# Performance work log

Hardware: AMD Instinct MI355X
Metric: run time of the kernel (lower is better)

Reference implementation:

```python
import jax, jax.numpy as jnp
import numpy as np

MAX_GRAD = 200.0
N_BLOCKS = 8

@jax.custom_jvp
def sqrt_bound(x):
    return jnp.sqrt(x)

@sqrt_bound.defjvp
def _sqrt_bound_jvp(primals, tangents):
    (x,), (xd,) = primals, tangents
    clipped = jnp.maximum(x, 1.0 / (4.0 * MAX_GRAD * MAX_GRAD))
    return jnp.sqrt(x), xd / (2.0 * jnp.sqrt(clipped))

def block_diag_linear(x, W, b):
    # x: [B,S,Din], W: [n_blocks, Din/n, Dout/n], b: [Dout]
    B, S, Din = x.shape
    n, blk_in, blk_out = W.shape
    xb = x.reshape(B, S, n, blk_in)
    y = jnp.einsum('bsnh,nhd->bsnd', xb, W).reshape(B, S, n * blk_out)
    return y + b

def _scan_combine(c1, c2):
    a1r, a1i, x1r, x1i = c1
    a2r, a2i, x2r, x2i = c2
    ar = a2r * a1r - a2i * a1i
    ai = a2r * a1i + a2i * a1r
    xr = a2r * x1r - a2i * x1i + x2r
    xi = a2r * x1i + a2i * x1r + x2i
    return (ar, ai, xr, xi)

def rglru_forward(x, a_real_param, a_imag_param, W_in, b_in, Wg_x, bg_x, Wg_a, bg_a, W_out, b_out):
    # x: [B, S, d_in]
    x_h = jnp.einsum('bsd,dh->bsh', x, W_in) + b_in          # [B,S,d_hidden]
    gate_x = jax.nn.sigmoid(block_diag_linear(x_h, Wg_x, bg_x))  # [B,S,Dh]
    gate_a = jax.nn.sigmoid(block_diag_linear(x_h, Wg_a, bg_a))  # [B,S,Dh]
    log_a = -8.0 * gate_a * jax.nn.softplus(a_real_param)        # Re(log a)
    log_a_imag = a_imag_param * gate_a                           # Im(log a)
    mag = jnp.exp(log_a)
    a_re = mag * jnp.cos(log_a_imag)
    a_im = mag * jnp.sin(log_a_imag)
    a_sq = jnp.exp(2.0 * log_a)                                  # |a|^2
    Dh = log_a.shape[-1]
    # merged_to_complex: first half -> real part, second half -> imag part
    xr = x_h[..., :Dh]
    xi = x_h[..., Dh:]
    xr = gate_x * xr
    xi = gate_x * xi
    norm = sqrt_bound(1.0 - a_sq)                                # input normalization
    xr = norm * xr
    xi = norm * xi
    # linear recurrence h_t = a_t * h_{t-1} + x_t  (h0 = 0), parallel scan over seq axis
    _, _, hr, hi = jax.lax.associative_scan(_scan_combine, (a_re, a_im, xr, xi), axis=1)
    h = jnp.concatenate([hr, hi], axis=-1)                       # complex_to_merged
    h_last = jnp.concatenate([hr[:, -1], hi[:, -1]], axis=-1)    # [B, d_hidden]
    y = jnp.einsum('bsh,hd->bsd', h, W_out) + b_out              # Dense(d_in)
    return y, h_last

def setup_inputs() -> dict:
    key = jax.random.key(0)
    ks = jax.random.split(key, 10)
    B, S, d_in, d_hidden = 4, 4096, 2048, 2048
    Dh = d_hidden // 2
    blk_in, blk_out = d_hidden // N_BLOCKS, Dh // N_BLOCKS
    r_min, r_max, max_imag, eps = 0.9, 0.999, 0.1, 1e-8
    u1 = jax.random.uniform(ks[0], (Dh,))
    a_real = 0.5 * jnp.log(u1 * (r_max**2 - r_min**2) + r_min**2 + eps)
    a_real_param = jnp.log(jnp.exp(-a_real) - 1.0)
    a_imag_param = jnp.pi * max_imag * jax.random.uniform(ks[1], (Dh,))
    x = jax.random.normal(ks[2], (B, S, d_in), dtype=jnp.float32)
    W_in = jax.random.normal(ks[3], (d_in, d_hidden)) / np.sqrt(d_in)
    Wg_x = jax.random.normal(ks[4], (N_BLOCKS, blk_in, blk_out)) / np.sqrt(blk_in)
    Wg_a = jax.random.normal(ks[5], (N_BLOCKS, blk_in, blk_out)) / np.sqrt(blk_in)
    W_out = jax.random.normal(ks[6], (d_hidden, d_in)) / np.sqrt(d_hidden)
    return {
        'x': x,
        'a_real_param': a_real_param.astype(jnp.float32),
        'a_imag_param': a_imag_param.astype(jnp.float32),
        'W_in': W_in.astype(jnp.float32), 'b_in': jnp.zeros((d_hidden,), jnp.float32),
        'Wg_x': Wg_x.astype(jnp.float32), 'bg_x': jnp.zeros((Dh,), jnp.float32),
        'Wg_a': Wg_a.astype(jnp.float32), 'bg_a': jnp.zeros((Dh,), jnp.float32),
        'W_out': W_out.astype(jnp.float32), 'b_out': jnp.zeros((d_in,), jnp.float32),
    }

def reference(x, a_real_param, a_imag_param, W_in, b_in, Wg_x, bg_x, Wg_a, bg_a, W_out, b_out):
    return rglru_forward(x, a_real_param, a_imag_param, W_in, b_in, Wg_x, bg_x, Wg_a, bg_a, W_out, b_out)
```

## Files before the change

### kernel.cpp

```cpp
#include <hip/hip_runtime.h>
#include <hip/hip_bf16.h>


typedef unsigned short u16;
typedef unsigned int u32;
typedef unsigned long long u64;
typedef __attribute__((ext_vector_type(8))) short short8;
typedef __attribute__((ext_vector_type(4))) float floatx4;

#define DEV __device__ __forceinline__

DEV float bf2f(u16 u) { union { u32 i; float f; } v; v.i = ((u32)u) << 16; return v.f; }
DEV u16 f2bf(float f) {
  union { float f; u32 i; } v; v.f = f;
  u32 r = v.i + 0x7fffu + ((v.i >> 16) & 1u);
  return (u16)(r >> 16);
}
DEV float sigmoidf_(float x) { return 1.f / (1.f + __expf(-x)); }

#if __has_builtin(__builtin_amdgcn_global_load_lds)
#define USE_ASYNC_LDS 1
#endif

DEV void cp16(const void* g, void* l) {
#if defined(USE_ASYNC_LDS) && defined(__HIP_DEVICE_COMPILE__)
  __builtin_amdgcn_global_load_lds((const __attribute__((address_space(1))) u32*)g,
                                   (__attribute__((address_space(3))) u32*)l, 16, 0, 0);
#else
  *(short8*)l = *(const short8*)g;
#endif
}
#define WAIT_VM() asm volatile("s_waitcnt vmcnt(0)" ::: "memory")

__global__ __launch_bounds__(256) void convert_f32_bf16(
    const float* __restrict__ src, u16* __restrict__ dst, long n) {
  long i = ((long)blockIdx.x * 256 + threadIdx.x) * 8;
  if (i >= n) return;
  float4 a = *(const float4*)(src + i);
  float4 b = *(const float4*)(src + i + 4);
  union { u16 u[8]; short8 v; } o;
  o.u[0] = f2bf(a.x); o.u[1] = f2bf(a.y); o.u[2] = f2bf(a.z); o.u[3] = f2bf(a.w);
  o.u[4] = f2bf(b.x); o.u[5] = f2bf(b.y); o.u[6] = f2bf(b.z); o.u[7] = f2bf(b.w);
  *(short8*)(dst + i) = o.v;
}

__global__ __launch_bounds__(256) void transpose_f32_bf16(
    const float* __restrict__ src, u16* __restrict__ dst, int R, int C,
    long sBatch, long dBatch) {
  __shared__ u16 tile[32][33];
  const int n = blockIdx.z;
  src += (long)n * sBatch;
  dst += (long)n * dBatch;
  const int c0 = blockIdx.x * 32, r0 = blockIdx.y * 32;
  const int tx = threadIdx.x, ty = threadIdx.y;
#pragma unroll
  for (int i = 0; i < 32; i += 8)
    tile[ty + i][tx] = f2bf(src[(long)(r0 + ty + i) * C + c0 + tx]);
  __syncthreads();
#pragma unroll
  for (int i = 0; i < 32; i += 8) dst[(long)(c0 + ty + i) * R + r0 + tx] = tile[tx][ty + i];
}

#define MQ(MH, NH)                                                                   \
  {                                                                                  \
    _Pragma("unroll") for (int mi = 0; mi < 4; ++mi)                                 \
        _Pragma("unroll") for (int nj = 0; nj < 2; ++nj) {                           \
      acc[(MH)*4 + mi][(NH)*2 + nj] = __builtin_amdgcn_mfma_f32_16x16x32_bf16(       \
          af[(MH)*4 + mi][0], bf[(NH)*2 + nj][0], acc[(MH)*4 + mi][(NH)*2 + nj],     \
          0, 0, 0);                                                                  \
      acc[(MH)*4 + mi][(NH)*2 + nj] = __builtin_amdgcn_mfma_f32_16x16x32_bf16(       \
          af[(MH)*4 + mi][1], bf[(NH)*2 + nj][1], acc[(MH)*4 + mi][(NH)*2 + nj],     \
          0, 0, 0);                                                                  \
    }                                                                                \
  }

#define AOFF(mi, k2) ((((wr << 7) + ((mi) << 4) + lm) << 6) + (((((k2) << 2) + lq) ^ sz) << 3))
#define BOFF(nj, k2) ((((wc << 6) + ((nj) << 4) + lm) << 6) + (((((k2) << 2) + lq) ^ sz) << 3))

template <typename OutT>
__global__ __launch_bounds__(512, 2) void gemm256_bt_bias(
    const u16* __restrict__ A, const u16* __restrict__ BT,
    const float* __restrict__ bias, OutT* __restrict__ C, int M, int N, int K) {
  __shared__ __align__(16) u16 As[2 * 16384];
  __shared__ __align__(16) u16 Bs[2 * 16384];
  const int mt = M >> 8;
  const int cpx = gridDim.x >> 3;
  const int bid = blockIdx.x;
  const int wg = (bid & 7) * cpx + (bid >> 3);
  const int bm = wg % mt, bn = wg / mt;
  const int m0 = bm << 8, n0 = bn << 8;
  const int tid = threadIdx.x;
  const int lane = tid & 63, wid = tid >> 6;
  const int wr = wid >> 2, wc = wid & 3;
  const int lq = lane >> 4, lm = lane & 15;
  const int sz = lm & 7;
  const int NT = K >> 6;

  auto stage = [&](int h) {
    int t = h >> 2, j = h & 3;
    const u16* src;
    u16* dst;
    if (j < 2) { src = A + (size_t)(m0 + (j << 7)) * K; dst = As; }
    else       { src = BT + (size_t)(n0 + ((j & 1) << 7)) * K; dst = Bs; }
    dst += ((t & 1) << 14) + ((j & 1) << 13);
    const size_t kb = (size_t)(t << 6);
#pragma unroll
    for (int l = 0; l < 2; ++l) {
      int slot = (l << 9) + tid;
      int row = slot >> 3;
      int gch = (slot & 7) ^ (row & 7);
      cp16(src + (size_t)row * K + kb + (gch << 3), (char*)dst + slot * 16);
    }
  };

  floatx4 acc[8][4];
#pragma unroll
  for (int i = 0; i < 8; ++i)
#pragma unroll
    for (int j = 0; j < 4; ++j) { acc[i][j].x = 0.f; acc[i][j].y = 0.f; acc[i][j].z = 0.f; acc[i][j].w = 0.f; }
  short8 af[8][2], bf[4][2];

#pragma unroll
  for (int h = 0; h < 7; ++h)
    if (h < 4 * NT) stage(h);
  asm volatile("s_waitcnt vmcnt(6)" ::: "memory");
  __builtin_amdgcn_s_barrier();

  for (int T = 0; T < NT; ++T) {
    const u16* Asb = As + ((T & 1) << 14);
    const u16* Bsb = Bs + ((T & 1) << 14);
    const int hb = (T << 2) + 7;
#pragma unroll
    for (int mi = 0; mi < 8; ++mi) {
      af[mi][0] = *(const short8*)(Asb + AOFF(mi, 0));
      af[mi][1] = *(const short8*)(Asb + AOFF(mi, 1));
    }
#pragma unroll
    for (int nj = 0; nj < 2; ++nj) {
      bf[nj][0] = *(const short8*)(Bsb + BOFF(nj, 0));
      bf[nj][1] = *(const short8*)(Bsb + BOFF(nj, 1));
    }
    if (hb < 4 * NT) stage(hb);
    __builtin_amdgcn_s_barrier();
    asm volatile("s_waitcnt lgkmcnt(0)" ::: "memory");
    __builtin_amdgcn_sched_barrier(0);
    __builtin_amdgcn_s_setprio(1);
    MQ(0, 0);
    __builtin_amdgcn_s_setprio(0);
    __builtin_amdgcn_s_barrier();
#pragma unroll
    for (int nj = 2; nj < 4; ++nj) {
      bf[nj][0] = *(const short8*)(Bsb + BOFF(nj, 0));
      bf[nj][1] = *(const short8*)(Bsb + BOFF(nj, 1));
    }
    if (hb + 1 < 4 * NT) stage(hb + 1);
    __builtin_amdgcn_s_barrier();
    asm volatile("s_waitcnt lgkmcnt(0)" ::: "memory");
    __builtin_amdgcn_sched_barrier(0);
    __builtin_amdgcn_s_setprio(1);
    MQ(0, 1);
    __builtin_amdgcn_s_setprio(0);
    __builtin_amdgcn_s_barrier();
    if (hb + 2 < 4 * NT) stage(hb + 2);
    __builtin_amdgcn_s_barrier();
    __builtin_amdgcn_s_setprio(1);
    MQ(1, 0);
    __builtin_amdgcn_s_setprio(0);
    __builtin_amdgcn_s_barrier();
    if (hb + 3 < 4 * NT) stage(hb + 3);
    __builtin_amdgcn_s_barrier();
    __builtin_amdgcn_s_setprio(1);
    MQ(1, 1);
    __builtin_amdgcn_s_setprio(0);
    if (T == NT - 2) { asm volatile("s_waitcnt vmcnt(0)" ::: "memory"); }
    else if (T < NT - 2) { asm volatile("s_waitcnt vmcnt(6)" ::: "memory"); }
    __builtin_amdgcn_s_barrier();
  }

  float bv[4];
#pragma unroll
  for (int nj = 0; nj < 4; ++nj) bv[nj] = bias[n0 + (wc << 6) + nj * 16 + lm];
  float* Cs = (float*)As;
#pragma unroll
  for (int s = 0; s < 4; ++s) {
    __syncthreads();
    if (wr == (s >> 1)) {
#pragma unroll
      for (int mi2 = 0; mi2 < 4; ++mi2) {
        const int mi = ((s & 1) << 2) + mi2;
#pragma unroll
        for (int nj = 0; nj < 4; ++nj)
#pragma unroll
          for (int rr = 0; rr < 4; ++rr)
            Cs[(mi2 * 16 + lq * 4 + rr) * 256 + (wc << 6) + nj * 16 + lm] =
                acc[mi][nj][rr] + bv[nj];
      }
    }
    __syncthreads();
#pragma unroll
    for (int w = 0; w < 8; ++w) {
      int fi = (w << 9) + tid;
      int rl = fi >> 6, cc = fi & 63;
      float4 v = *(const float4*)&Cs[rl * 256 + (cc << 2)];
      size_t grow = (size_t)(m0 + (s << 6) + rl) * N + n0 + (cc << 2);
      if constexpr (sizeof(OutT) == 2) {
        union { u16 u[4]; u64 q; } o;
        o.u[0] = f2bf(v.x); o.u[1] = f2bf(v.y); o.u[2] = f2bf(v.z); o.u[3] = f2bf(v.w);
        *(u64*)((u16*)C + grow) = o.q;
      } else {
        *(float4*)((float*)C + grow) = v;
      }
    }
  }
}

__global__ __launch_bounds__(256, 2) void gate_elem_kernel(
    const u16* __restrict__ xh, const u16* __restrict__ wgt,
    const float* __restrict__ bgx, const float* __restrict__ bga,
    const float* __restrict__ arp,
    float* __restrict__ ga_out, u16* __restrict__ xr_out, u16* __restrict__ xi_out) {
  __shared__ __align__(16) u16 As[128 * 64];
  __shared__ __align__(16) u16 Bs[256 * 64];

  const int m0 = blockIdx.x << 7;
  const int blk = blockIdx.y;
  const int tid = threadIdx.x;
  const int lane = tid & 63, wid = tid >> 6;
  const int wm = (wid & 1) << 6, wn = (wid >> 1) << 6;
  const int lq = lane >> 4, lm = lane & 15;

  floatx4 acc[4][8];
#pragma unroll
  for (int i = 0; i < 4; ++i)
#pragma unroll
    for (int j = 0; j < 8; ++j) { acc[i][j].x = 0.f; acc[i][j].y = 0.f; acc[i][j].z = 0.f; acc[i][j].w = 0.f; }

  const u16* Ag = xh + (size_t)m0 * 2048 + blk * 256;
  const u16* Bg = wgt + (size_t)blk * 65536;

  for (int kt = 0; kt < 256; kt += 64) {
#pragma unroll
    for (int j = 0; j < 4; ++j) {
      int slot = (j << 8) + tid;
      int row = slot >> 3, ch = slot & 7;
      int gch = ch ^ (row & 7);
      cp16(Ag + (size_t)row * 2048 + kt + (gch << 3), (char*)As + slot * 16);
    }
#pragma unroll
    for (int j = 0; j < 8; ++j) {
      int slot = (j << 8) + tid;
      int row = slot >> 3, ch = slot & 7;
      int gch = ch ^ (row & 7);
      cp16(Bg + (size_t)row * 256 + kt + (gch << 3), (char*)Bs + slot * 16);
    }
    WAIT_VM();
    __syncthreads();
#pragma unroll
    for (int kk = 0; kk < 64; kk += 32) {
      const int lc = (kk >> 3) + lq;
      short8 af[4], bfr[8];
#pragma unroll
      for (int mi = 0; mi < 4; ++mi) {
        int r = wm + mi * 16 + lm;
        af[mi] = *(const short8*)&As[r * 64 + ((lc ^ (r & 7)) << 3)];
      }
#pragma unroll
      for (int ni = 0; ni < 8; ++ni) {
        int r = (ni < 4) ? (wn + ni * 16 + lm) : (128 + wn + (ni - 4) * 16 + lm);
        bfr[ni] = *(const short8*)&Bs[r * 64 + ((lc ^ (r & 7)) << 3)];
      }
#pragma unroll
      for (int mi = 0; mi < 4; ++mi)
#pragma unroll
        for (int ni = 0; ni < 8; ++ni)
          acc[mi][ni] = __builtin_amdgcn_mfma_f32_16x16x32_bf16(af[mi], bfr[ni], acc[mi][ni], 0, 0, 0);
    }
    __syncthreads();
  }

#pragma unroll
  for (int ni = 0; ni < 4; ++ni) {
    const int c = (blk << 7) + wn + ni * 16 + lm;
    const float bxv = bgx[c], bav = bga[c];
    const float sp = log1pf(__expf(arp[c]));
#pragma unroll
    for (int mi = 0; mi < 4; ++mi) {
      const size_t rowg0 = (size_t)m0 + wm + mi * 16 + lq * 4;
#pragma unroll
      for (int r = 0; r < 4; ++r) {
        const size_t rowg = rowg0 + r;
        float gxv = sigmoidf_(acc[mi][ni][r] + bxv);
        float gav = sigmoidf_(acc[mi][ni + 4][r] + bav);
        float mag = __expf(-8.f * gav * sp);
        float norm = sqrtf(fmaxf(1.f - mag * mag, 0.f));
        float f = norm * gxv;
        ga_out[rowg * 1024 + c] = gav;
        xr_out[rowg * 1024 + c] = f2bf(f * bf2f(xh[rowg * 2048 + c]));
        xi_out[rowg * 1024 + c] = f2bf(f * bf2f(xh[rowg * 2048 + 1024 + c]));
      }
    }
  }
}

__global__ __launch_bounds__(256) void scan_pass1(
    const float* __restrict__ ga, const u16* __restrict__ xr, const u16* __restrict__ xi,
    const float* __restrict__ arp, const float* __restrict__ aip,
    float* __restrict__ Ar, float* __restrict__ Ai,
    float* __restrict__ Xr, float* __restrict__ Xi) {
  int tid = blockIdx.x * 256 + threadIdx.x;
  int c = tid & 1023;
  int chunk = (tid >> 10) & 63;
  int b = tid >> 16;
  float sp = log1pf(__expf(arp[c]));
  float aim = aip[c];
  size_t base = ((size_t)b * 4096 + chunk * 64) * 1024 + c;
  float Arr = 1.f, Aii = 0.f, Xrr = 0.f, Xii = 0.f;
#pragma unroll 4
  for (int i = 0; i < 64; ++i) {
    size_t idx = base + (size_t)i * 1024;
    float g = ga[idx];
    float mag = __expf(-8.f * g * sp);
    float s, co;
    __sincosf(aim * g, &s, &co);
    float ar = mag * co, ai = mag * s;
    float nxr = ar * Xrr - ai * Xii + bf2f(xr[idx]);
    float nxi = ar * Xii + ai * Xrr + bf2f(xi[idx]);
    Xrr = nxr; Xii = nxi;
    float nar = ar * Arr - ai * Aii;
    float nai = ar * Aii + ai * Arr;
    Arr = nar; Aii = nai;
  }
  Ar[tid] = Arr; Ai[tid] = Aii; Xr[tid] = Xrr; Xi[tid] = Xii;
}

__global__ __launch_bounds__(256) void scan_pass2(
    const float* __restrict__ Ar, const float* __restrict__ Ai,
    const float* __restrict__ Xr, const float* __restrict__ Xi,
    float* __restrict__ Hr, float* __restrict__ Hi) {
  int tid = blockIdx.x * 256 + threadIdx.x;
  int c = tid & 1023, b = tid >> 10;
  float hr = 0.f, hi = 0.f;
  for (int j = 0; j < 64; ++j) {
    int idx = (b << 16) + (j << 10) + c;
    Hr[idx] = hr; Hi[idx] = hi;
    float ar = Ar[idx], ai = Ai[idx];
    float nhr = ar * hr - ai * hi + Xr[idx];
    float nhi = ar * hi + ai * hr + Xi[idx];
    hr = nhr; hi = nhi;
  }
}

__global__ __launch_bounds__(256) void scan_pass3(
    const float* __restrict__ ga, const u16* __restrict__ xr, const u16* __restrict__ xi,
    const float* __restrict__ arp, const float* __restrict__ aip,
    const float* __restrict__ Hr, const float* __restrict__ Hi,
    u16* __restrict__ h_out, float* __restrict__ tail) {
  int tid = blockIdx.x * 256 + threadIdx.x;
  int c = tid & 1023;
  int chunk = (tid >> 10) & 63;
  int b = tid >> 16;
  float sp = log1pf(__expf(arp[c]));
  float aim = aip[c];
  size_t row0 = (size_t)b * 4096 + chunk * 64;
  size_t base = row0 * 1024 + c;
  float hr = Hr[tid], hi = Hi[tid];
#pragma unroll 4
  for (int i = 0; i < 64; ++i) {
    size_t idx = base + (size_t)i * 1024;
    float g = ga[idx];
    float mag = __expf(-8.f * g * sp);
    float s, co;
    __sincosf(aim * g, &s, &co);
    float ar = mag * co, ai = mag * s;
    float nhr = ar * hr - ai * hi + bf2f(xr[idx]);
    float nhi = ar * hi + ai * hr + bf2f(xi[idx]);
    hr = nhr; hi = nhi;
    size_t r = row0 + i;
    h_out[r * 2048 + c] = f2bf(hr);
    h_out[r * 2048 + 1024 + c] = f2bf(hi);
  }
  if (chunk == 63) {
    tail[(size_t)b * 2048 + c] = hr;
    tail[(size_t)b * 2048 + 1024 + c] = hi;
  }
}

static const size_t OFF_XH = 0;
static const size_t OFF_GA = 67108864;
static const size_t OFF_XR = 134217728;
static const size_t OFF_XI = 167772160;
static const size_t OFF_WIT = 201326592;
static const size_t OFF_WOT = 209715200;
static const size_t OFF_WGT = 218103808;
static const size_t OFF_AGR = 219152384;
static const size_t OFF_AGI = 220200960;
static const size_t OFF_AXR = 221249536;
static const size_t OFF_AXI = 222298112;
static const size_t OFF_HPR = 223346688;
static const size_t OFF_HPI = 224395264;

extern "C" void kernel_launch(void* const* d_in, const int* in_sizes, int n_in,
                              void* d_out, int out_size, void* d_ws, size_t ws_size,
                              hipStream_t stream) {
  const float* x    = (const float*)d_in[0];
  const float* arp  = (const float*)d_in[1];
  const float* aip  = (const float*)d_in[2];
  const float* W_in = (const float*)d_in[3];
  const float* b_in = (const float*)d_in[4];
  const float* Wg_x = (const float*)d_in[5];
  const float* bg_x = (const float*)d_in[6];
  const float* Wg_a = (const float*)d_in[7];
  const float* bg_a = (const float*)d_in[8];
  const float* W_out = (const float*)d_in[9];
  const float* b_out = (const float*)d_in[10];

  char* ws = (char*)d_ws;
  u16* XH = (u16*)(ws + OFF_XH);
  u16* XB = (u16*)(ws + OFF_GA);
  float* GA = (float*)(ws + OFF_GA);
  u16* XR = (u16*)(ws + OFF_XR);
  u16* XI = (u16*)(ws + OFF_XI);
  u16* WIT = (u16*)(ws + OFF_WIT);
  u16* WOT = (u16*)(ws + OFF_WOT);
  u16* WGT = (u16*)(ws + OFF_WGT);
  float* AGR = (float*)(ws + OFF_AGR);
  float* AGI = (float*)(ws + OFF_AGI);
  float* AXR = (float*)(ws + OFF_AXR);
  float* AXI = (float*)(ws + OFF_AXI);
  float* HPR = (float*)(ws + OFF_HPR);
  float* HPI = (float*)(ws + OFF_HPI);

  float* y_out = (float*)d_out;
  float* h_last = (float*)d_out + (size_t)16384 * 2048;

  convert_f32_bf16<<<16384, 256, 0, stream>>>(x, XB, (long)16384 * 2048);

  dim3 tb(32, 8);
  transpose_f32_bf16<<<dim3(64, 64, 1), tb, 0, stream>>>(W_in, WIT, 2048, 2048, 0, 0);
  transpose_f32_bf16<<<dim3(64, 64, 1), tb, 0, stream>>>(W_out, WOT, 2048, 2048, 0, 0);
  transpose_f32_bf16<<<dim3(4, 8, 8), tb, 0, stream>>>(Wg_x, WGT, 256, 128, 32768, 65536);
  transpose_f32_bf16<<<dim3(4, 8, 8), tb, 0, stream>>>(Wg_a, WGT + 32768, 256, 128, 32768, 65536);

  gemm256_bt_bias<u16><<<512, 512, 0, stream>>>(XB, WIT, b_in, XH, 16384, 2048, 2048);
  gate_elem_kernel<<<dim3(128, 8), 256, 0, stream>>>(XH, WGT, bg_x, bg_a, arp, GA, XR, XI);
  scan_pass1<<<1024, 256, 0, stream>>>(GA, XR, XI, arp, aip, AGR, AGI, AXR, AXI);
  scan_pass2<<<16, 256, 0, stream>>>(AGR, AGI, AXR, AXI, HPR, HPI);
  scan_pass3<<<1024, 256, 0, stream>>>(GA, XR, XI, arp, aip, HPR, HPI, XH , h_last);
  gemm256_bt_bias<float><<<512, 512, 0, stream>>>(XH, WOT, b_out, y_out, 16384, 2048, 2048);
}
```

Baseline: 731.1 us.

## Software-pipeline LDS fragment reads across GEMM quarter-steps and pad epilogue stride

Restructures the 256x256 GEMM main loop so LDS fragment reads for the next quadrant, and for the next k-tile, are issued while the current MFMA quadrant runs. Global-to-LDS staging of half-tiles is reordered and the vmcnt waits are adjusted to match. The epilogue staging buffer row stride is padded from 256 to 260 floats to reduce LDS bank conflicts. The intent is to hide LDS read latency behind MFMA work, at the cost of more complex wait and barrier accounting that could introduce races if the counts are wrong.

```diff
diff --git a/kernel.cpp b/kernel.cpp
--- a/kernel.cpp
+++ b/kernel.cpp
@@ -31,6 +31,7 @@
 #endif
 }
 #define WAIT_VM() asm volatile("s_waitcnt vmcnt(0)" ::: "memory")
+#define LGKM0()  do { asm volatile("s_waitcnt lgkmcnt(0)" ::: "memory"); __builtin_amdgcn_sched_barrier(0); } while (0)
 
 __global__ __launch_bounds__(256) void convert_f32_bf16(
     const float* __restrict__ src, u16* __restrict__ dst, long n) {
@@ -77,12 +78,28 @@
 #define AOFF(mi, k2) ((((wr << 7) + ((mi) << 4) + lm) << 6) + (((((k2) << 2) + lq) ^ sz) << 3))
 #define BOFF(nj, k2) ((((wc << 6) + ((nj) << 4) + lm) << 6) + (((((k2) << 2) + lq) ^ sz) << 3))
 
+#define RD_A4(m0_, p)                                                   \
+  {                                                                     \
+    _Pragma("unroll") for (int mi = (m0_); mi < (m0_) + 4; ++mi) {      \
+      af[mi][0] = *(const short8*)((p) + AOFF(mi, 0));                  \
+      af[mi][1] = *(const short8*)((p) + AOFF(mi, 1));                  \
+    }                                                                   \
+  }
+#define RD_B2(n0_, p)                                                   \
+  {                                                                     \
+    _Pragma("unroll") for (int nj = (n0_); nj < (n0_) + 2; ++nj) {      \
+      bf[nj][0] = *(const short8*)((p) + BOFF(nj, 0));                  \
+      bf[nj][1] = *(const short8*)((p) + BOFF(nj, 1));                  \
+    }                                                                   \
+  }
+
 template <typename OutT>
 __global__ __launch_bounds__(512, 2) void gemm256_bt_bias(
     const u16* __restrict__ A, const u16* __restrict__ BT,
     const float* __restrict__ bias, OutT* __restrict__ C, int M, int N, int K) {
-  __shared__ __align__(16) u16 As[2 * 16384];
-  __shared__ __align__(16) u16 Bs[2 * 16384];
+  __shared__ __align__(16) u16 SM[65536];
+  u16* As = SM;
+  u16* Bs = SM + 32768;
   const int mt = M >> 8;
   const int cpx = gridDim.x >> 3;
   const int bid = blockIdx.x;
@@ -96,8 +113,7 @@
   const int sz = lm & 7;
   const int NT = K >> 6;
 
-  auto stage = [&](int h) {
-    int t = h >> 2, j = h & 3;
+  auto stageH = [&](int t, int j) {
     const u16* src;
     u16* dst;
     if (j < 2) { src = A + (size_t)(m0 + (j << 7)) * K; dst = As; }
@@ -120,67 +136,61 @@
     for (int j = 0; j < 4; ++j) { acc[i][j].x = 0.f; acc[i][j].y = 0.f; acc[i][j].z = 0.f; acc[i][j].w = 0.f; }
   short8 af[8][2], bf[4][2];
 
-#pragma unroll
-  for (int h = 0; h < 7; ++h)
-    if (h < 4 * NT) stage(h);
+  stageH(0, 0); stageH(0, 2); stageH(0, 1); stageH(0, 3);
+  stageH(1, 0); stageH(1, 2); stageH(1, 1);
   asm volatile("s_waitcnt vmcnt(6)" ::: "memory");
   __builtin_amdgcn_s_barrier();
+  RD_A4(0, As);
+  RD_B2(0, Bs);
 
   for (int T = 0; T < NT; ++T) {
-    const u16* Asb = As + ((T & 1) << 14);
-    const u16* Bsb = Bs + ((T & 1) << 14);
-    const int hb = (T << 2) + 7;
-#pragma unroll
-    for (int mi = 0; mi < 8; ++mi) {
-      af[mi][0] = *(const short8*)(Asb + AOFF(mi, 0));
-      af[mi][1] = *(const short8*)(Asb + AOFF(mi, 1));
-    }
-#pragma unroll
-    for (int nj = 0; nj < 2; ++nj) {
-      bf[nj][0] = *(const short8*)(Bsb + BOFF(nj, 0));
-      bf[nj][1] = *(const short8*)(Bsb + BOFF(nj, 1));
-    }
-    if (hb < 4 * NT) stage(hb);
-    __builtin_amdgcn_s_barrier();
-    asm volatile("s_waitcnt lgkmcnt(0)" ::: "memory");
-    __builtin_amdgcn_sched_barrier(0);
+    const u16* ca = As + ((T & 1) << 14);
+    const u16* cb = Bs + ((T & 1) << 14);
+    const u16* na = As + (((T + 1) & 1) << 14);
+    const u16* nb = Bs + (((T + 1) & 1) << 14);
+    const bool haveN1 = (T + 1 < NT), haveN2 = (T + 2 < NT);
+    if (haveN1) stageH(T + 1, 3);
+    __builtin_amdgcn_s_barrier();
+    LGKM0();
+    RD_B2(2, cb);
     __builtin_amdgcn_s_setprio(1);
     MQ(0, 0);
     __builtin_amdgcn_s_setprio(0);
     __builtin_amdgcn_s_barrier();
-#pragma unroll
-    for (int nj = 2; nj < 4; ++nj) {
-      bf[nj][0] = *(const short8*)(Bsb + BOFF(nj, 0));
-      bf[nj][1] = *(const short8*)(Bsb + BOFF(nj, 1));
-    }
-    if (hb + 1 < 4 * NT) stage(hb + 1);
-    __builtin_amdgcn_s_barrier();
-    asm volatile("s_waitcnt lgkmcnt(0)" ::: "memory");
-    __builtin_amdgcn_sched_barrier(0);
+    if (haveN2) stageH(T + 2, 0);
+    __builtin_amdgcn_s_barrier();
+    LGKM0();
+    RD_A4(4, ca);
     __builtin_amdgcn_s_setprio(1);
     MQ(0, 1);
     __builtin_amdgcn_s_setprio(0);
-    __builtin_amdgcn_s_barrier();
-    if (hb + 2 < 4 * NT) stage(hb + 2);
-    __builtin_amdgcn_s_barrier();
+    if (T < NT - 2) { asm volatile("s_waitcnt vmcnt(8)" ::: "memory"); }
+    else            { asm volatile("s_waitcnt vmcnt(0)" ::: "memory"); }
+    __builtin_amdgcn_s_barrier();
+    if (haveN2) stageH(T + 2, 2);
+    __builtin_amdgcn_s_barrier();
+    LGKM0();
+    if (haveN1) RD_A4(0, na);
     __builtin_amdgcn_s_setprio(1);
     MQ(1, 0);
     __builtin_amdgcn_s_setprio(0);
-    __builtin_amdgcn_s_barrier();
-    if (hb + 3 < 4 * NT) stage(hb + 3);
-    __builtin_amdgcn_s_barrier();
+    if (T < NT - 2) { asm volatile("s_waitcnt vmcnt(4)" ::: "memory"); }
+    else            { asm volatile("s_waitcnt vmcnt(0)" ::: "memory"); }
+    __builtin_amdgcn_s_barrier();
+    if (haveN2) stageH(T + 2, 1);
+    __builtin_amdgcn_s_barrier();
+    LGKM0();
+    if (haveN1) RD_B2(0, nb);
     __builtin_amdgcn_s_setprio(1);
     MQ(1, 1);
     __builtin_amdgcn_s_setprio(0);
-    if (T == NT - 2) { asm volatile("s_waitcnt vmcnt(0)" ::: "memory"); }
-    else if (T < NT - 2) { asm volatile("s_waitcnt vmcnt(6)" ::: "memory"); }
     __builtin_amdgcn_s_barrier();
   }
 
   float bv[4];
 #pragma unroll
   for (int nj = 0; nj < 4; ++nj) bv[nj] = bias[n0 + (wc << 6) + nj * 16 + lm];
-  float* Cs = (float*)As;
+  float* Cs = (float*)SM;
 #pragma unroll
   for (int s = 0; s < 4; ++s) {
     __syncthreads();
@@ -192,7 +202,7 @@
         for (int nj = 0; nj < 4; ++nj)
 #pragma unroll
           for (int rr = 0; rr < 4; ++rr)
-            Cs[(mi2 * 16 + lq * 4 + rr) * 256 + (wc << 6) + nj * 16 + lm] =
+            Cs[(mi2 * 16 + lq * 4 + rr) * 260 + (wc << 6) + nj * 16 + lm] =
                 acc[mi][nj][rr] + bv[nj];
       }
     }
@@ -201,7 +211,7 @@
     for (int w = 0; w < 8; ++w) {
       int fi = (w << 9) + tid;
       int rl = fi >> 6, cc = fi & 63;
-      float4 v = *(const float4*)&Cs[rl * 256 + (cc << 2)];
+      float4 v = *(const float4*)&Cs[rl * 260 + (cc << 2)];
       size_t grow = (size_t)(m0 + (s << 6) + rl) * N + n0 + (cc << 2);
       if constexpr (sizeof(OutT) == 2) {
         union { u16 u[4]; u64 q; } o;
```

Measured after the change: 711.4 us. 2.7% less time.

## Restructure GEMM main loop with interleaved LDS reads and compile-time K

Applied to the files above, without the earlier changes.

Rewrites the 256x256 bf16 GEMM mainloop to interleave LDS fragment reads, async global-to-LDS staging and MFMA quarters more finely. The two fragment reads per quarter are now spread across phases, with the next tile's A reads prefetched during the current tile. K becomes a template constant, so NT and address offsets are precomputed and the loop has a peeled tail. The epilogue staging buffer is padded to a 260-float stride to cut LDS bank conflicts. The tighter vmcnt and barrier choreography carries a risk of subtle race bugs.

```diff
diff --git a/kernel.cpp b/kernel.cpp
--- a/kernel.cpp
+++ b/kernel.cpp
@@ -31,6 +31,10 @@
 #endif
 }
 #define WAIT_VM() asm volatile("s_waitcnt vmcnt(0)" ::: "memory")
+#define LGKM0()  do { asm volatile("s_waitcnt lgkmcnt(0)" ::: "memory"); __builtin_amdgcn_sched_barrier(0); } while (0)
+#define BAR()    __builtin_amdgcn_s_barrier()
+#define VMC4()   asm volatile("s_waitcnt vmcnt(4)" ::: "memory")
+#define SETP(p)  __builtin_amdgcn_s_setprio(p)
 
 __global__ __launch_bounds__(256) void convert_f32_bf16(
     const float* __restrict__ src, u16* __restrict__ dst, long n) {
@@ -61,28 +65,41 @@
   for (int i = 0; i < 32; i += 8) dst[(long)(c0 + ty + i) * R + r0 + tx] = tile[tx][ty + i];
 }
 
-#define MQ(MH, NH)                                                                   \
+#define MQK(MH, NH)                                                                  \
   {                                                                                  \
     _Pragma("unroll") for (int mi = 0; mi < 4; ++mi)                                 \
-        _Pragma("unroll") for (int nj = 0; nj < 2; ++nj) {                           \
+        _Pragma("unroll") for (int nj = 0; nj < 2; ++nj)                             \
       acc[(MH)*4 + mi][(NH)*2 + nj] = __builtin_amdgcn_mfma_f32_16x16x32_bf16(       \
           af[(MH)*4 + mi][0], bf[(NH)*2 + nj][0], acc[(MH)*4 + mi][(NH)*2 + nj],     \
           0, 0, 0);                                                                  \
+    _Pragma("unroll") for (int mi = 0; mi < 4; ++mi)                                 \
+        _Pragma("unroll") for (int nj = 0; nj < 2; ++nj)                             \
       acc[(MH)*4 + mi][(NH)*2 + nj] = __builtin_amdgcn_mfma_f32_16x16x32_bf16(       \
           af[(MH)*4 + mi][1], bf[(NH)*2 + nj][1], acc[(MH)*4 + mi][(NH)*2 + nj],     \
           0, 0, 0);                                                                  \
+  }
+
+#define RDA(m0_, BO)                                                                 \
+  {                                                                                  \
+    _Pragma("unroll") for (int mi = (m0_); mi < (m0_) + 4; ++mi) {                   \
+      af[mi][0] = *(const short8*)((const char*)SM + ((aRd0 ^ (BO)) + mi * 2048));   \
+      af[mi][1] = *(const short8*)((const char*)SM + ((aRd1 ^ (BO)) + mi * 2048));   \
     }                                                                                \
   }
-
-#define AOFF(mi, k2) ((((wr << 7) + ((mi) << 4) + lm) << 6) + (((((k2) << 2) + lq) ^ sz) << 3))
-#define BOFF(nj, k2) ((((wc << 6) + ((nj) << 4) + lm) << 6) + (((((k2) << 2) + lq) ^ sz) << 3))
-
-template <typename OutT>
+#define RDB(n0_, BO)                                                                 \
+  {                                                                                  \
+    _Pragma("unroll") for (int nj = (n0_); nj < (n0_) + 2; ++nj) {                   \
+      bf[nj][0] = *(const short8*)((const char*)SM + ((bRd0 ^ (BO)) + nj * 2048));   \
+      bf[nj][1] = *(const short8*)((const char*)SM + ((bRd1 ^ (BO)) + nj * 2048));   \
+    }                                                                                \
+  }
+
+template <typename OutT, int KK>
 __global__ __launch_bounds__(512, 2) void gemm256_bt_bias(
     const u16* __restrict__ A, const u16* __restrict__ BT,
-    const float* __restrict__ bias, OutT* __restrict__ C, int M, int N, int K) {
-  __shared__ __align__(16) u16 As[2 * 16384];
-  __shared__ __align__(16) u16 Bs[2 * 16384];
+    const float* __restrict__ bias, OutT* __restrict__ C, int M, int N) {
+  constexpr int NT = KK >> 6;
+  __shared__ __align__(16) u16 SM[65536];
   const int mt = M >> 8;
   const int cpx = gridDim.x >> 3;
   const int bid = blockIdx.x;
@@ -94,24 +111,29 @@
   const int wr = wid >> 2, wc = wid & 3;
   const int lq = lane >> 4, lm = lane & 15;
   const int sz = lm & 7;
-  const int NT = K >> 6;
-
-  auto stage = [&](int h) {
-    int t = h >> 2, j = h & 3;
-    const u16* src;
-    u16* dst;
-    if (j < 2) { src = A + (size_t)(m0 + (j << 7)) * K; dst = As; }
-    else       { src = BT + (size_t)(n0 + ((j & 1) << 7)) * K; dst = Bs; }
-    dst += ((t & 1) << 14) + ((j & 1) << 13);
-    const size_t kb = (size_t)(t << 6);
-#pragma unroll
-    for (int l = 0; l < 2; ++l) {
-      int slot = (l << 9) + tid;
-      int row = slot >> 3;
-      int gch = (slot & 7) ^ (row & 7);
-      cp16(src + (size_t)row * K + kb + (gch << 3), (char*)dst + slot * 16);
-    }
+
+  u32 goffA0, goffA1, goffB0, goffB1;
+  u32 lofA0, lofA1, lofB0, lofB1;
+  {
+    const int rowl = tid >> 3, gch = (tid & 7) ^ (rowl & 7);
+    goffA0 = (u32)(((size_t)(m0 + rowl) * KK + (gch << 3)) * 2);
+    goffA1 = (u32)(((size_t)(m0 + 128 + rowl) * KK + (gch << 3)) * 2);
+    goffB0 = (u32)(((size_t)(n0 + rowl) * KK + (gch << 3)) * 2);
+    goffB1 = (u32)(((size_t)(n0 + 128 + rowl) * KK + (gch << 3)) * 2);
+    const u32 sl = (u32)tid * 16;
+    lofA0 = sl; lofA1 = sl + 16384; lofB0 = sl + 65536; lofB1 = sl + 81920;
+  }
+  const u32 aRd0 = (u32)((((wr << 7) + lm) << 7) + ((lq ^ sz) << 4));
+  const u32 aRd1 = aRd0 ^ 64u;
+  const u32 bRd0 = (u32)(65536 + (((wc << 6) + lm) << 7) + ((lq ^ sz) << 4));
+  const u32 bRd1 = bRd0 ^ 64u;
+
+  auto stage2 = [&](u32 go, const char* base, u32 lo, u32 bo) {
+    cp16(base + go, (char*)SM + (lo ^ bo));
+    cp16(base + go + 64 * KK * 2, (char*)SM + ((lo ^ bo) + 8192));
   };
+#define SBA(t) ((const char*)A + ((size_t)(t) << 7))
+#define SBB(t) ((const char*)BT + ((size_t)(t) << 7))
 
   floatx4 acc[8][4];
 #pragma unroll
@@ -120,67 +142,66 @@
     for (int j = 0; j < 4; ++j) { acc[i][j].x = 0.f; acc[i][j].y = 0.f; acc[i][j].z = 0.f; acc[i][j].w = 0.f; }
   short8 af[8][2], bf[4][2];
 
-#pragma unroll
-  for (int h = 0; h < 7; ++h)
-    if (h < 4 * NT) stage(h);
+  stage2(goffA0, SBA(0), lofA0, 0);
+  stage2(goffB0, SBB(0), lofB0, 0);
+  stage2(goffA1, SBA(0), lofA1, 0);
+  stage2(goffB1, SBB(0), lofB1, 0);
+  stage2(goffA0, SBA(1), lofA0, 0x8000u);
+  stage2(goffB0, SBB(1), lofB0, 0x8000u);
+  stage2(goffA1, SBA(1), lofA1, 0x8000u);
   asm volatile("s_waitcnt vmcnt(6)" ::: "memory");
-  __builtin_amdgcn_s_barrier();
-
-  for (int T = 0; T < NT; ++T) {
-    const u16* Asb = As + ((T & 1) << 14);
-    const u16* Bsb = Bs + ((T & 1) << 14);
-    const int hb = (T << 2) + 7;
-#pragma unroll
-    for (int mi = 0; mi < 8; ++mi) {
-      af[mi][0] = *(const short8*)(Asb + AOFF(mi, 0));
-      af[mi][1] = *(const short8*)(Asb + AOFF(mi, 1));
-    }
-#pragma unroll
-    for (int nj = 0; nj < 2; ++nj) {
-      bf[nj][0] = *(const short8*)(Bsb + BOFF(nj, 0));
-      bf[nj][1] = *(const short8*)(Bsb + BOFF(nj, 1));
-    }
-    if (hb < 4 * NT) stage(hb);
-    __builtin_amdgcn_s_barrier();
-    asm volatile("s_waitcnt lgkmcnt(0)" ::: "memory");
-    __builtin_amdgcn_sched_barrier(0);
-    __builtin_amdgcn_s_setprio(1);
-    MQ(0, 0);
-    __builtin_amdgcn_s_setprio(0);
-    __builtin_amdgcn_s_barrier();
-#pragma unroll
-    for (int nj = 2; nj < 4; ++nj) {
-      bf[nj][0] = *(const short8*)(Bsb + BOFF(nj, 0));
-      bf[nj][1] = *(const short8*)(Bsb + BOFF(nj, 1));
-    }
-    if (hb + 1 < 4 * NT) stage(hb + 1);
-    __builtin_amdgcn_s_barrier();
-    asm volatile("s_waitcnt lgkmcnt(0)" ::: "memory");
-    __builtin_amdgcn_sched_barrier(0);
-    __builtin_amdgcn_s_setprio(1);
-    MQ(0, 1);
-    __builtin_amdgcn_s_setprio(0);
-    __builtin_amdgcn_s_barrier();
-    if (hb + 2 < 4 * NT) stage(hb + 2);
-    __builtin_amdgcn_s_barrier();
-    __builtin_amdgcn_s_setprio(1);
-    MQ(1, 0);
-    __builtin_amdgcn_s_setprio(0);
-    __builtin_amdgcn_s_barrier();
-    if (hb + 3 < 4 * NT) stage(hb + 3);
-    __builtin_amdgcn_s_barrier();
-    __builtin_amdgcn_s_setprio(1);
-    MQ(1, 1);
-    __builtin_amdgcn_s_setprio(0);
-    if (T == NT - 2) { asm volatile("s_waitcnt vmcnt(0)" ::: "memory"); }
-    else if (T < NT - 2) { asm volatile("s_waitcnt vmcnt(6)" ::: "memory"); }
-    __builtin_amdgcn_s_barrier();
-  }
+  BAR();
+  RDA(0, 0u);
+  RDB(0, 0u);
+
+  for (int T = 0; T < NT - 2; ++T) {
+    const u32 bo = (u32)((T & 1) << 15), bq = bo ^ 0x8000u;
+    stage2(goffB1, SBB(T + 1), lofB1, bq);
+    BAR(); LGKM0();
+    RDB(2, bo);
+    SETP(1); MQK(0, 0); SETP(0);
+    BAR();
+    stage2(goffA0, SBA(T + 2), lofA0, bo);
+    BAR(); LGKM0();
+    RDA(4, bo);
+    SETP(1); MQK(0, 1); SETP(0);
+    VMC4();
+    BAR();
+    stage2(goffB0, SBB(T + 2), lofB0, bo);
+    BAR(); LGKM0();
+    RDA(0, bq);
+    SETP(1); MQK(1, 0); SETP(0);
+    VMC4();
+    BAR();
+    stage2(goffA1, SBA(T + 2), lofA1, bo);
+    BAR(); LGKM0();
+    RDB(0, bq);
+    SETP(1); MQK(1, 1); SETP(0);
+    BAR();
+  }
+  {
+    const int T = NT - 2;
+    const u32 bo = (u32)((T & 1) << 15), bq = bo ^ 0x8000u;
+    stage2(goffB1, SBB(T + 1), lofB1, bq);
+    BAR(); LGKM0(); RDB(2, bo); SETP(1); MQK(0, 0); SETP(0); BAR();
+    BAR(); LGKM0(); RDA(4, bo); SETP(1); MQK(0, 1); SETP(0); WAIT_VM(); BAR();
+    BAR(); LGKM0(); RDA(0, bq); SETP(1); MQK(1, 0); SETP(0); BAR();
+    BAR(); LGKM0(); RDB(0, bq); SETP(1); MQK(1, 1); SETP(0); BAR();
+  }
+  {
+    const u32 bo = (u32)(((NT - 1) & 1) << 15);
+    BAR(); LGKM0(); RDB(2, bo); SETP(1); MQK(0, 0); SETP(0); BAR();
+    BAR(); LGKM0(); RDA(4, bo); SETP(1); MQK(0, 1); SETP(0); BAR();
+    BAR(); LGKM0(); SETP(1); MQK(1, 0); SETP(0); BAR();
+    BAR(); LGKM0(); SETP(1); MQK(1, 1); SETP(0); BAR();
+  }
+#undef SBA
+#undef SBB
 
   float bv[4];
 #pragma unroll
   for (int nj = 0; nj < 4; ++nj) bv[nj] = bias[n0 + (wc << 6) + nj * 16 + lm];
-  float* Cs = (float*)As;
+  float* Cs = (float*)SM;
 #pragma unroll
   for (int s = 0; s < 4; ++s) {
     __syncthreads();
@@ -192,7 +213,7 @@
         for (int nj = 0; nj < 4; ++nj)
 #pragma unroll
           for (int rr = 0; rr < 4; ++rr)
-            Cs[(mi2 * 16 + lq * 4 + rr) * 256 + (wc << 6) + nj * 16 + lm] =
+            Cs[(mi2 * 16 + lq * 4 + rr) * 260 + (wc << 6) + nj * 16 + lm] =
                 acc[mi][nj][rr] + bv[nj];
       }
     }
@@ -201,7 +222,7 @@
     for (int w = 0; w < 8; ++w) {
       int fi = (w << 9) + tid;
       int rl = fi >> 6, cc = fi & 63;
-      float4 v = *(const float4*)&Cs[rl * 256 + (cc << 2)];
+      float4 v = *(const float4*)&Cs[rl * 260 + (cc << 2)];
       size_t grow = (size_t)(m0 + (s << 6) + rl) * N + n0 + (cc << 2);
       if constexpr (sizeof(OutT) == 2) {
         union { u16 u[4]; u64 q; } o;
@@ -441,10 +462,10 @@
   transpose_f32_bf16<<<dim3(4, 8, 8), tb, 0, stream>>>(Wg_x, WGT, 256, 128, 32768, 65536);
   transpose_f32_bf16<<<dim3(4, 8, 8), tb, 0, stream>>>(Wg_a, WGT + 32768, 256, 128, 32768, 65536);
 
-  gemm256_bt_bias<u16><<<512, 512, 0, stream>>>(XB, WIT, b_in, XH, 16384, 2048, 2048);
+  gemm256_bt_bias<u16, 2048><<<512, 512, 0, stream>>>(XB, WIT, b_in, XH, 16384, 2048);
   gate_elem_kernel<<<dim3(128, 8), 256, 0, stream>>>(XH, WGT, bg_x, bg_a, arp, GA, XR, XI);
   scan_pass1<<<1024, 256, 0, stream>>>(GA, XR, XI, arp, aip, AGR, AGI, AXR, AXI);
   scan_pass2<<<16, 256, 0, stream>>>(AGR, AGI, AXR, AXI, HPR, HPI);
   scan_pass3<<<1024, 256, 0, stream>>>(GA, XR, XI, arp, aip, HPR, HPI, XH , h_last);
-  gemm256_bt_bias<float><<<512, 512, 0, stream>>>(XH, WOT, b_out, y_out, 16384, 2048, 2048);
-}
+  gemm256_bt_bias<float, 2048><<<512, 512, 0, stream>>>(XH, WOT, b_out, y_out, 16384, 2048);
+}
```

Result: faster. 706.9 us (-3.3%).
